# Kernel tuning notes

Measured on AMD Instinct MI355X. Metric: run time of the kernel, lower is better.

## Reference

```python
import jax, jax.numpy as jnp
import numpy as np

N_POINTS_TOTAL = 1_000_000
FEAT_DIM = 64
B = 128            # number of point clouds (segments)
LATENT_DIM = 512
NUM_POINTS = 2048  # decoder output points per cloud
EPS = 1e-5


def setup_inputs() -> dict:
    key = jax.random.key(0)
    ks = jax.random.split(key, 12)
    s = 0.02
    feat = jax.random.normal(ks[0], (N_POINTS_TOTAL, FEAT_DIM), dtype=jnp.float32)
    # sorted segment ids in [0, B); with 1M points and 128 segments every segment is nonempty
    batch = jnp.sort(jax.random.randint(ks[1], (N_POINTS_TOTAL,), 0, B, dtype=jnp.int64))
    return {
        "feat": feat,
        "batch": batch,
        "ln_g": jnp.ones((FEAT_DIM,), jnp.float32),
        "ln_b": jnp.zeros((FEAT_DIM,), jnp.float32),
        # Linear weights stored [in, out] (transposed vs torch)
        "proj_w": jax.random.normal(ks[2], (FEAT_DIM, LATENT_DIM), jnp.float32) * s,
        "proj_b": jnp.zeros((LATENT_DIM,), jnp.float32),
        "w1": jax.random.normal(ks[3], (LATENT_DIM, 256), jnp.float32) * s,
        "b1": jnp.zeros((256,), jnp.float32),
        "w2": jax.random.normal(ks[4], (256, 512), jnp.float32) * s,
        "b2": jnp.zeros((512,), jnp.float32),
        "w3": jax.random.normal(ks[5], (512, NUM_POINTS * 3), jnp.float32) * s,
        "b3": jnp.zeros((NUM_POINTS * 3,), jnp.float32),
    }


def reference(feat, batch, ln_g, ln_b, proj_w, proj_b, w1, b1, w2, b2, w3, b3):
    # Ragged per-cloud max pool: replaces the per-sample Python loop with one segment-max.
    pooled = jax.ops.segment_max(feat, batch, num_segments=B)  # [B, 64]
    # LayerNorm(64)
    mu = jnp.mean(pooled, axis=-1, keepdims=True)
    var = jnp.mean(jnp.square(pooled - mu), axis=-1, keepdims=True)
    x = (pooled - mu) * jax.lax.rsqrt(var + EPS) * ln_g + ln_b
    # proj + decoder MLP
    latent = x @ proj_w + proj_b                               # [B, 512]
    h = jax.nn.relu(latent @ w1 + b1)                          # [B, 256]
    h = jax.nn.relu(h @ w2 + b2)                               # [B, 512]
    out = h @ w3 + b3                                          # [B, NUM_POINTS*3]
    return out.reshape(-1, NUM_POINTS, 3)
```

## Files before the change

kernel.cpp:

```cpp
#include <hip/hip_runtime.h>
#include <hip/hip_bf16.h>

#define N_POINTS 1000000
#define FEAT 64
#define BSEG 128
#define EPS 1e-5f
#define CHUNK 2048
#define NBLK_SEG ((N_POINTS + CHUNK - 1) / CHUNK)

__device__ __forceinline__ unsigned ordered_enc(float f) {
    unsigned u = __float_as_uint(f);
    return (u & 0x80000000u) ? ~u : (u | 0x80000000u);
}
__device__ __forceinline__ float ordered_dec(unsigned v) {
    unsigned u = (v & 0x80000000u) ? (v & 0x7fffffffu) : ~v;
    return __uint_as_float(u);
}

#define ENC_NEG_INF 0x007FFFFFu

__global__ void k_init(unsigned* __restrict__ pool) {
    int i = blockIdx.x * blockDim.x + threadIdx.x;
    if (i < BSEG * FEAT) pool[i] = ENC_NEG_INF;
}

__global__ __launch_bounds__(256) void k_segmax(const float4* __restrict__ feat,
                                                const int* __restrict__ batch,
                                                unsigned* __restrict__ pool) {
    __shared__ unsigned short sb[CHUNK];
    __shared__ unsigned spool[4 * FEAT];
    const int t = threadIdx.x;
    const int base = blockIdx.x * CHUNK;
    int rem = N_POINTS - base;
    if (rem > CHUNK) rem = CHUNK;

    for (int i = t; i < CHUNK; i += 256)
        sb[i] = (i < rem) ? (unsigned short)batch[base + i] : (unsigned short)0xFFFF;
    spool[t] = 0u;
    __syncthreads();

    const int seg0 = sb[0];
    const int q = t & 15;
    const int r = t >> 4;

    float4 m = make_float4(-INFINITY, -INFINITY, -INFINITY, -INFINITY);
    int cur = -1;

    auto flush = [&](int seg, float4 mm) {
        unsigned e0 = ordered_enc(mm.x), e1 = ordered_enc(mm.y);
        unsigned e2 = ordered_enc(mm.z), e3 = ordered_enc(mm.w);
        int slot = seg - seg0;
        if (slot >= 0 && slot < 4) {
            unsigned* p = &spool[slot * FEAT + q * 4];
            atomicMax(&p[0], e0); atomicMax(&p[1], e1);
            atomicMax(&p[2], e2); atomicMax(&p[3], e3);
        } else {
            unsigned* p = &pool[seg * FEAT + q * 4];
            atomicMax(&p[0], e0); atomicMax(&p[1], e1);
            atomicMax(&p[2], e2); atomicMax(&p[3], e3);
        }
    };

    for (int i = r; i < rem; i += 16) {
        int seg = sb[i];
        if (seg != cur) {
            if (cur >= 0) flush(cur, m);
            cur = seg;
            m = make_float4(-INFINITY, -INFINITY, -INFINITY, -INFINITY);
        }
        float4 v = feat[(base + i) * 16 + q];
        m.x = fmaxf(m.x, v.x); m.y = fmaxf(m.y, v.y);
        m.z = fmaxf(m.z, v.z); m.w = fmaxf(m.w, v.w);
    }
    if (cur >= 0) flush(cur, m);
    __syncthreads();

    unsigned v = spool[t];
    if (v != 0u) {
        int slot = t >> 6;
        int seg = seg0 + slot;
        atomicMax(&pool[seg * FEAT + (t & 63)], v);
    }
}

__global__ __launch_bounds__(256) void k_mlp(const unsigned* __restrict__ pool,
                                             const float* __restrict__ ln_g,
                                             const float* __restrict__ ln_b,
                                             const float* __restrict__ pw,
                                             const float* __restrict__ pb,
                                             const float* __restrict__ w1,
                                             const float* __restrict__ b1,
                                             const float* __restrict__ w2,
                                             const float* __restrict__ b2,
                                             float* __restrict__ h2out) {
    __shared__ float xn[64];
    __shared__ float lat[512];
    __shared__ float h1s[256];
    const int b = blockIdx.x, t = threadIdx.x;

    if (t < 64) {
        float x = ordered_dec(pool[b * 64 + t]);
        float s = x;
        #pragma unroll
        for (int off = 32; off > 0; off >>= 1) s += __shfl_xor(s, off, 64);
        float mu = s * (1.0f / 64.0f);
        float d = x - mu;
        float s2 = d * d;
        #pragma unroll
        for (int off = 32; off > 0; off >>= 1) s2 += __shfl_xor(s2, off, 64);
        float var = s2 * (1.0f / 64.0f);
        xn[t] = d * rsqrtf(var + EPS) * ln_g[t] + ln_b[t];
    }
    __syncthreads();

    {
        float a0 = pb[t], a1 = pb[t + 256];
        #pragma unroll 8
        for (int j = 0; j < 64; ++j) {
            float xj = xn[j];
            a0 = fmaf(xj, pw[j * 512 + t], a0);
            a1 = fmaf(xj, pw[j * 512 + t + 256], a1);
        }
        lat[t] = a0; lat[t + 256] = a1;
    }
    __syncthreads();

    {
        float a = b1[t];
        #pragma unroll 8
        for (int j = 0; j < 512; ++j)
            a = fmaf(lat[j], w1[j * 256 + t], a);
        h1s[t] = fmaxf(a, 0.0f);
    }
    __syncthreads();

    {
        float a0 = b2[t], a1 = b2[t + 256];
        #pragma unroll 8
        for (int j = 0; j < 256; ++j) {
            float hj = h1s[j];
            a0 = fmaf(hj, w2[j * 512 + t], a0);
            a1 = fmaf(hj, w2[j * 512 + t + 256], a1);
        }
        h2out[b * 512 + t] = fmaxf(a0, 0.0f);
        h2out[b * 512 + t + 256] = fmaxf(a1, 0.0f);
    }
}

#define FS 132
__global__ __launch_bounds__(256) void k_final(const float* __restrict__ h2,
                                               const float* __restrict__ w3,
                                               const float* __restrict__ b3,
                                               float* __restrict__ out) {
    __shared__ float sh[64 * FS];
    const int t = threadIdx.x;
    const int cp = blockIdx.x, rp = blockIdx.y;
    const int rbase = rp * 64;
    const int tx = t & 15, ty = t >> 4;
    const int c = cp * 64 + tx * 4;
    const int r0 = ty * 4;

    float4 bias = *(const float4*)&b3[c];
    float4 acc[4] = {bias, bias, bias, bias};

    const float4* h2g = (const float4*)h2;
    for (int kc = 0; kc < 512; kc += 128) {
        __syncthreads();
        #pragma unroll
        for (int it = 0; it < 8; ++it) {
            int idx = it * 256 + t;
            int r = idx >> 5;
            int kq = idx & 31;
            float4 v = h2g[(rbase + r) * 128 + (kc >> 2) + kq];
            *(float4*)&sh[r * FS + kq * 4] = v;
        }
        __syncthreads();
        for (int kb = 0; kb < 128; kb += 4) {
            float4 a[4];
            #pragma unroll
            for (int i = 0; i < 4; ++i)
                a[i] = *(const float4*)&sh[(r0 + i) * FS + kb];
            #pragma unroll
            for (int kk = 0; kk < 4; ++kk) {
                float4 w = *(const float4*)&w3[(kc + kb + kk) * 6144 + c];
                #pragma unroll
                for (int i = 0; i < 4; ++i) {
                    float e = (kk == 0) ? a[i].x : (kk == 1) ? a[i].y
                            : (kk == 2) ? a[i].z : a[i].w;
                    acc[i].x = fmaf(e, w.x, acc[i].x);
                    acc[i].y = fmaf(e, w.y, acc[i].y);
                    acc[i].z = fmaf(e, w.z, acc[i].z);
                    acc[i].w = fmaf(e, w.w, acc[i].w);
                }
            }
        }
    }
    #pragma unroll
    for (int i = 0; i < 4; ++i)
        *(float4*)&out[(rbase + r0 + i) * 6144 + c] = acc[i];
}

extern "C" void kernel_launch(void* const* d_in, const int* in_sizes, int n_in,
                              void* d_out, int out_size, void* d_ws, size_t ws_size,
                              hipStream_t stream) {
    const float* feat  = (const float*)d_in[0];
    const int*   batch = (const int*)d_in[1];
    const float* ln_g  = (const float*)d_in[2];
    const float* ln_b  = (const float*)d_in[3];
    const float* pw    = (const float*)d_in[4];
    const float* pb    = (const float*)d_in[5];
    const float* w1    = (const float*)d_in[6];
    const float* b1    = (const float*)d_in[7];
    const float* w2    = (const float*)d_in[8];
    const float* b2    = (const float*)d_in[9];
    const float* w3    = (const float*)d_in[10];
    const float* b3    = (const float*)d_in[11];
    float* out = (float*)d_out;

    unsigned* pool = (unsigned*)d_ws;
    float* h2buf = (float*)d_ws + BSEG * FEAT;

    k_init<<<(BSEG * FEAT + 255) / 256, 256, 0, stream>>>(pool);
    k_segmax<<<NBLK_SEG, 256, 0, stream>>>((const float4*)feat, batch, pool);
    k_mlp<<<BSEG, 256, 0, stream>>>(pool, ln_g, ln_b, pw, pb, w1, b1, w2, b2, h2buf);
    k_final<<<dim3(96, 2), 256, 0, stream>>>(h2buf, w3, b3, out);
}
```

Measured before the change: 518.0 us.

## Halve segmax chunk with 2 float4 per thread; one block per column strip in final GEMM

The segment-max kernel now uses 1024-point chunks, which doubles the block count. Each thread loads two float4s per point (8 threads per row), and loads are issued before the segment check. The final GEMM drops the split over two row groups: each of 96 blocks of 512 threads covers all 128 rows. This makes each w3 element load once from global memory instead of twice, at the cost of fewer blocks and a larger shared tile. Per-thread work in the final kernel stays at 4x4 outputs.

```diff
diff --git a/kernel.cpp b/kernel.cpp
--- a/kernel.cpp
+++ b/kernel.cpp
@@ -5,7 +5,7 @@
 #define FEAT 64
 #define BSEG 128
 #define EPS 1e-5f
-#define CHUNK 2048
+#define CHUNK 1024
 #define NBLK_SEG ((N_POINTS + CHUNK - 1) / CHUNK)
 
 __device__ __forceinline__ unsigned ordered_enc(float f) {
@@ -40,46 +40,51 @@
     __syncthreads();
 
     const int seg0 = sb[0];
-    const int q = t & 15;
-    const int r = t >> 4;
-
-    float4 m = make_float4(-INFINITY, -INFINITY, -INFINITY, -INFINITY);
+    const int q = t & 7;
+    const int r = t >> 3;
+
+    float4 m0 = make_float4(-INFINITY, -INFINITY, -INFINITY, -INFINITY);
+    float4 m1 = m0;
     int cur = -1;
 
-    auto flush = [&](int seg, float4 mm) {
-        unsigned e0 = ordered_enc(mm.x), e1 = ordered_enc(mm.y);
-        unsigned e2 = ordered_enc(mm.z), e3 = ordered_enc(mm.w);
+    auto flush = [&](int seg, float4 a, float4 b) {
+        unsigned e[8] = { ordered_enc(a.x), ordered_enc(a.y), ordered_enc(a.z), ordered_enc(a.w),
+                          ordered_enc(b.x), ordered_enc(b.y), ordered_enc(b.z), ordered_enc(b.w) };
         int slot = seg - seg0;
         if (slot >= 0 && slot < 4) {
-            unsigned* p = &spool[slot * FEAT + q * 4];
-            atomicMax(&p[0], e0); atomicMax(&p[1], e1);
-            atomicMax(&p[2], e2); atomicMax(&p[3], e3);
+            unsigned* p = &spool[slot * FEAT + q * 8];
+            #pragma unroll
+            for (int j = 0; j < 8; ++j) atomicMax(&p[j], e[j]);
         } else {
-            unsigned* p = &pool[seg * FEAT + q * 4];
-            atomicMax(&p[0], e0); atomicMax(&p[1], e1);
-            atomicMax(&p[2], e2); atomicMax(&p[3], e3);
+            unsigned* p = &pool[seg * FEAT + q * 8];
+            #pragma unroll
+            for (int j = 0; j < 8; ++j) atomicMax(&p[j], e[j]);
         }
     };
 
-    for (int i = r; i < rem; i += 16) {
+    for (int i = r; i < rem; i += 32) {
+        const float4* p = &feat[(size_t)(base + i) * 16 + q * 2];
+        float4 v0 = p[0];
+        float4 v1 = p[1];
         int seg = sb[i];
         if (seg != cur) {
-            if (cur >= 0) flush(cur, m);
+            if (cur >= 0) flush(cur, m0, m1);
             cur = seg;
-            m = make_float4(-INFINITY, -INFINITY, -INFINITY, -INFINITY);
-        }
-        float4 v = feat[(base + i) * 16 + q];
-        m.x = fmaxf(m.x, v.x); m.y = fmaxf(m.y, v.y);
-        m.z = fmaxf(m.z, v.z); m.w = fmaxf(m.w, v.w);
-    }
-    if (cur >= 0) flush(cur, m);
+            m0 = make_float4(-INFINITY, -INFINITY, -INFINITY, -INFINITY);
+            m1 = m0;
+        }
+        m0.x = fmaxf(m0.x, v0.x); m0.y = fmaxf(m0.y, v0.y);
+        m0.z = fmaxf(m0.z, v0.z); m0.w = fmaxf(m0.w, v0.w);
+        m1.x = fmaxf(m1.x, v1.x); m1.y = fmaxf(m1.y, v1.y);
+        m1.z = fmaxf(m1.z, v1.z); m1.w = fmaxf(m1.w, v1.w);
+    }
+    if (cur >= 0) flush(cur, m0, m1);
     __syncthreads();
 
     unsigned v = spool[t];
     if (v != 0u) {
         int slot = t >> 6;
-        int seg = seg0 + slot;
-        atomicMax(&pool[seg * FEAT + (t & 63)], v);
+        atomicMax(&pool[(seg0 + slot) * FEAT + (t & 63)], v);
     }
 }
 
@@ -147,17 +152,16 @@
     }
 }
 
-#define FS 132
-__global__ __launch_bounds__(256) void k_final(const float* __restrict__ h2,
+#define RS 136
+__global__ __launch_bounds__(512) void k_final(const float* __restrict__ h2,
                                                const float* __restrict__ w3,
                                                const float* __restrict__ b3,
                                                float* __restrict__ out) {
-    __shared__ float sh[64 * FS];
+    __shared__ float h2s[128 * RS];
     const int t = threadIdx.x;
-    const int cp = blockIdx.x, rp = blockIdx.y;
-    const int rbase = rp * 64;
-    const int tx = t & 15, ty = t >> 4;
-    const int c = cp * 64 + tx * 4;
+    const int tx = t & 15;
+    const int ty = t >> 4;
+    const int c = blockIdx.x * 64 + tx * 4;
     const int r0 = ty * 4;
 
     float4 bias = *(const float4*)&b3[c];
@@ -168,36 +172,33 @@
         __syncthreads();
         #pragma unroll
         for (int it = 0; it < 8; ++it) {
-            int idx = it * 256 + t;
-            int r = idx >> 5;
+            int idx = it * 512 + t;
+            int rr = idx >> 5;
             int kq = idx & 31;
-            float4 v = h2g[(rbase + r) * 128 + (kc >> 2) + kq];
-            *(float4*)&sh[r * FS + kq * 4] = v;
+            float4 v = h2g[rr * 128 + (kc >> 2) + kq];
+            *(float4*)&h2s[rr * RS + kq * 4] = v;
         }
         __syncthreads();
-        for (int kb = 0; kb < 128; kb += 4) {
-            float4 a[4];
-            #pragma unroll
-            for (int i = 0; i < 4; ++i)
-                a[i] = *(const float4*)&sh[(r0 + i) * FS + kb];
-            #pragma unroll
-            for (int kk = 0; kk < 4; ++kk) {
-                float4 w = *(const float4*)&w3[(kc + kb + kk) * 6144 + c];
-                #pragma unroll
-                for (int i = 0; i < 4; ++i) {
-                    float e = (kk == 0) ? a[i].x : (kk == 1) ? a[i].y
-                            : (kk == 2) ? a[i].z : a[i].w;
-                    acc[i].x = fmaf(e, w.x, acc[i].x);
-                    acc[i].y = fmaf(e, w.y, acc[i].y);
-                    acc[i].z = fmaf(e, w.z, acc[i].z);
-                    acc[i].w = fmaf(e, w.w, acc[i].w);
-                }
-            }
+        #pragma unroll 4
+        for (int k = 0; k < 128; ++k) {
+            float4 w = *(const float4*)&w3[(size_t)(kc + k) * 6144 + c];
+            float a0 = h2s[(r0 + 0) * RS + k];
+            float a1 = h2s[(r0 + 1) * RS + k];
+            float a2 = h2s[(r0 + 2) * RS + k];
+            float a3 = h2s[(r0 + 3) * RS + k];
+            acc[0].x = fmaf(a0, w.x, acc[0].x); acc[0].y = fmaf(a0, w.y, acc[0].y);
+            acc[0].z = fmaf(a0, w.z, acc[0].z); acc[0].w = fmaf(a0, w.w, acc[0].w);
+            acc[1].x = fmaf(a1, w.x, acc[1].x); acc[1].y = fmaf(a1, w.y, acc[1].y);
+            acc[1].z = fmaf(a1, w.z, acc[1].z); acc[1].w = fmaf(a1, w.w, acc[1].w);
+            acc[2].x = fmaf(a2, w.x, acc[2].x); acc[2].y = fmaf(a2, w.y, acc[2].y);
+            acc[2].z = fmaf(a2, w.z, acc[2].z); acc[2].w = fmaf(a2, w.w, acc[2].w);
+            acc[3].x = fmaf(a3, w.x, acc[3].x); acc[3].y = fmaf(a3, w.y, acc[3].y);
+            acc[3].z = fmaf(a3, w.z, acc[3].z); acc[3].w = fmaf(a3, w.w, acc[3].w);
         }
     }
     #pragma unroll
     for (int i = 0; i < 4; ++i)
-        *(float4*)&out[(rbase + r0 + i) * 6144 + c] = acc[i];
+        *(float4*)&out[(size_t)(r0 + i) * 6144 + c] = acc[i];
 }
 
 extern "C" void kernel_launch(void* const* d_in, const int* in_sizes, int n_in,
@@ -223,5 +224,5 @@
     k_init<<<(BSEG * FEAT + 255) / 256, 256, 0, stream>>>(pool);
     k_segmax<<<NBLK_SEG, 256, 0, stream>>>((const float4*)feat, batch, pool);
     k_mlp<<<BSEG, 256, 0, stream>>>(pool, ln_g, ln_b, pw, pb, w1, b1, w2, b2, h2buf);
-    k_final<<<dim3(96, 2), 256, 0, stream>>>(h2buf, w3, b3, out);
-}
+    k_final<<<96, 512, 0, stream>>>(h2buf, w3, b3, out);
+}
```

Result: faster. 503.1 us (-2.9%).
